# Kernel optimization log

Hardware: AMD Instinct MI355X
Metric: run time of the kernel (lower is better)

Reference implementation:

```python
import jax, jax.numpy as jnp
import numpy as np

LOSS_WEIGHT = 1.0

# Zero-padded shifts implementing PyTorch cross-correlation stencils.
# _shift_w(x, +1)[..., j] = x[..., j+1] (zero outside), etc.

def _shift_w(x, s):
    if s == 1:
        return jnp.pad(x[..., 1:], ((0, 0), (0, 0), (0, 1)))
    return jnp.pad(x[..., :-1], ((0, 0), (0, 0), (1, 0)))


def _shift_h(x, s):
    if s == 1:
        return jnp.pad(x[..., 1:, :], ((0, 0), (0, 1), (0, 0)))
    return jnp.pad(x[..., :-1, :], ((0, 0), (1, 0), (0, 0)))


def _curvature_loss(prob):
    # prob: [B, H, W]. Fused stencil chain equivalent to the 7 tiny conv2d calls.
    lap = (_shift_h(prob, 1) + _shift_h(prob, -1)
           + _shift_w(prob, 1) + _shift_w(prob, -1) - 4.0 * prob)
    gx = _shift_w(lap, 1) - _shift_w(lap, -1)          # dx = [-1, 0, 1]
    gy = _shift_h(lap, 1) - _shift_h(lap, -1)          # dy = [-1, 0, 1]^T
    hxx = 2.0 * gx - _shift_w(gx, 1) - _shift_w(gx, -1)  # dxx = [-1, 2, -1]
    hyy = 2.0 * gy - _shift_h(gy, 1) - _shift_h(gy, -1)  # dyy = [-1, 2, -1]^T
    hxy = _shift_w(gx, 1) - _shift_w(gx, -1)
    numerator = hxx * (1.0 + gy) ** 2 - 2.0 * hxy * gx * gy + hyy * (1.0 + gx) ** 2
    denominator = 2.0 * (1.0 + gx ** 2 + gy ** 2) ** 1.5
    curvature = numerator / denominator
    neg_curv = jnp.maximum(-curvature, 0.0)
    s = jnp.sum(neg_curv, axis=(1, 2))                              # [B]
    c = jnp.sum(neg_curv != 0, axis=(1, 2)).astype(prob.dtype)      # [B]
    # per-sample masked mean, skipped when no negative curvature
    per_sample = jnp.where(c > 0, s / jnp.maximum(c, 1.0), 0.0)
    return jnp.sum(per_sample)


def setup_inputs() -> dict:
    key = jax.random.key(0)
    k1, k2 = jax.random.split(key)
    pred = jax.random.normal(k1, (8, 4, 1024, 1024), dtype=jnp.float32)
    target = jax.random.randint(k2, (8, 1024, 1024), 0, 4, dtype=jnp.int64)
    return {"pred": pred, "target": target}


def reference(pred, target):
    # softmax=True path; num_classes == 4 branch of the original forward
    p = jax.nn.softmax(pred, axis=1)
    prob_1 = p[:, 1]
    prob_2 = p[:, 1] + p[:, 2]
    prob_3 = p[:, 3]
    loss = (_curvature_loss(prob_1) + _curvature_loss(prob_2)
            + _curvature_loss(prob_3))
    return loss * LOSS_WEIGHT
```

## Files before the change

### kernel.cpp

```cpp
#include <hip/hip_runtime.h>


namespace {
constexpr int H = 1024, W = 1024, B = 8;
constexpr int VALID = 120;
constexpr int NSTRIPS = 9;
constexpr int RCHUNK = 16;
constexpr int NCHUNKS = H / RCHUNK;
constexpr int WPB = 4;
constexpr int NTHREADS = 64 * WPB;
constexpr size_t HW = (size_t)H * W;
}

using v2f = __attribute__((ext_vector_type(2))) float;

__device__ __forceinline__ v2f mk2(float a, float b) {
    v2f r; r.x = a; r.y = b; return r;
}

__device__ __forceinline__ float dpp_left(float x) {
    return __builtin_bit_cast(float,
        __builtin_amdgcn_update_dpp(0, __builtin_bit_cast(int, x),
                                    0x138 , 0xf, 0xf, false));
}
__device__ __forceinline__ float dpp_right(float x) {
    return __builtin_bit_cast(float,
        __builtin_amdgcn_update_dpp(0, __builtin_bit_cast(int, x),
                                    0x130 , 0xf, 0xf, false));
}

__global__ void zero_ws_kernel(unsigned int* ws) {
    if (threadIdx.x < 48) ws[threadIdx.x] = 0u;
}

template <bool RE>
__device__ __forceinline__ void load_row4(const float* __restrict__ basep, int row,
                                          v2f o[4]) {
    const int rc = RE ? min(max(row, 0), H - 1) : row;
    const float* p = basep + (size_t)rc * W;
    o[0] = *(const v2f*)p;
    o[1] = *(const v2f*)(p + HW);
    o[2] = *(const v2f*)(p + 2 * HW);
    o[3] = *(const v2f*)(p + 3 * HW);
}

template <bool EDGE>
__device__ __forceinline__ void softmax_pair(const v2f x[4], bool ok0, bool ok1,
                                             v2f p[3]) {
    const float e0x = __expf(x[0].x), e1x = __expf(x[1].x);
    const float e2x = __expf(x[2].x), e3x = __expf(x[3].x);
    const float e0y = __expf(x[0].y), e1y = __expf(x[1].y);
    const float e2y = __expf(x[2].y), e3y = __expf(x[3].y);
    const float ix = __builtin_amdgcn_rcpf(e0x + e1x + e2x + e3x);
    const float iy = __builtin_amdgcn_rcpf(e0y + e1y + e2y + e3y);
    if (EDGE) {
        p[0] = mk2(ok0 ? e1x * ix : 0.f,          ok1 ? e1y * iy : 0.f);
        p[1] = mk2(ok0 ? (e1x + e2x) * ix : 0.f,  ok1 ? (e1y + e2y) * iy : 0.f);
        p[2] = mk2(ok0 ? e3x * ix : 0.f,          ok1 ? e3y * iy : 0.f);
    } else {
        p[0] = mk2(e1x * ix,          e1y * iy);
        p[1] = mk2((e1x + e2x) * ix,  (e1y + e2y) * iy);
        p[2] = mk2(e3x * ix,          e3y * iy);
    }
}

template <bool CE, bool RE>
__device__ __forceinline__ void sweep(const float* __restrict__ pred,
                                      int b, int strip, int chunk, int lane,
                                      v2f sacc[3], unsigned int cacc0[3],
                                      unsigned int cacc1[3]) {
    const int r0 = chunk * RCHUNK;
    const int li0 = 2 * lane;
    const int col0 = strip * VALID - 4 + li0;
    const int col1 = col0 + 1;
    const int colC = CE ? min(max(col0, 0), W - 2) : col0;
    const float* basep = pred + (size_t)b * 4 * HW + colC;

    const bool cOK0 = !CE || ((unsigned)col0 < (unsigned)W);
    const bool cOK1 = !CE || ((unsigned)col1 < (unsigned)W);
    const bool aOK0 = (li0 >= 4) && (li0 <= 123) && cOK0;
    const bool aOK1 = (li0 + 1 >= 4) && (li0 + 1 <= 123) && cOK1;
    const v2f aM = mk2(aOK0 ? 1.f : 0.f, aOK1 ? 1.f : 0.f);
    const v2f gxpM = mk2((!CE || (col0 + 1 < W)) ? 1.f : 0.f,
                         (!CE || (col1 + 1 < W)) ? 1.f : 0.f);
    const v2f gxmM = mk2((!CE || (col0 >= 1)) ? 1.f : 0.f,
                         (!CE || (col1 >= 1)) ? 1.f : 0.f);

    v2f P[5][3];
    v2f L[5][3];
    v2f Rr[2][4];

    {
        v2f t[4];
        load_row4<RE>(basep, r0 - 3, t);
        const bool ok = !RE || ((unsigned)(r0 - 3) < (unsigned)H);
        softmax_pair<CE || RE>(t, ok && cOK0, ok && cOK1, P[3]);
        load_row4<RE>(basep, r0 - 2, t);
        const bool ok2 = !RE || ((unsigned)(r0 - 2) < (unsigned)H);
        softmax_pair<CE || RE>(t, ok2 && cOK0, ok2 && cOK1, P[4]);
    }
    load_row4<RE>(basep, r0 - 1, Rr[0]);
    load_row4<RE>(basep, r0, Rr[1]);

    for (int m = 0; m < 2; ++m) {
#pragma unroll
        for (int u = 0; u < 10; ++u) {
            const int y = r0 - 4 + m * 10 + u;
            const bool pok = !RE || ((unsigned)(y + 3) < (unsigned)H);
            softmax_pair<CE || RE>(Rr[u % 2], pok && cOK0, pok && cOK1, P[u % 5]);
            load_row4<RE>(basep, y + 5, Rr[u % 2]);
            const bool lok = !RE || ((unsigned)(y + 2) < (unsigned)H);
#pragma unroll
            for (int f = 0; f < 3; ++f) {
                const v2f top = P[(u + 3) % 5][f];
                const v2f mid = P[(u + 4) % 5][f];
                const v2f bot = P[u % 5][f];
                const float lft = dpp_left(mid.y);
                const float rgt = dpp_right(mid.x);
                const v2f horiz = mk2(lft, mid.x) + mk2(mid.y, rgt);
                const v2f l = top + bot + horiz - 4.f * mid;
                if (CE || RE) {
                    L[u % 5][f] = mk2((lok && cOK0) ? l.x : 0.f,
                                      (lok && cOK1) ? l.y : 0.f);
                } else {
                    L[u % 5][f] = l;
                }
            }
            if (m > 0 || u >= 4) {
                const float gypM = (!RE || (y + 1 < H)) ? 1.f : 0.f;
                const float gymM = (!RE || (y >= 1)) ? 1.f : 0.f;
#pragma unroll
                for (int f = 0; f < 3; ++f) {
                    const v2f lm2 = L[(u + 1) % 5][f];
                    const v2f lm1 = L[(u + 2) % 5][f];
                    const v2f lc  = L[(u + 3) % 5][f];
                    const v2f lp1 = L[(u + 4) % 5][f];
                    const v2f lp2 = L[u % 5][f];
                    const float A  = dpp_left(lc.y);
                    const float Bm = dpp_left(lc.x);
                    const float Bp = dpp_right(lc.x);
                    const float Cc = dpp_right(lc.y);
                    const v2f c   = lc;
                    const v2f gx  = mk2(lc.y, Bp) - mk2(A, lc.x);
                    const v2f gy  = lp1 - lm1;
                    const v2f gxp = (mk2(Bp, Cc) - c) * gxpM;
                    const v2f gxm = (c - mk2(Bm, A)) * gxmM;
                    const v2f gyp = (lp2 - c) * gypM;
                    const v2f gym = (c - lm2) * gymM;
                    const v2f hxx = 2.f * gx - gxp - gxm;
                    const v2f hxy = gxp - gxm;
                    const v2f hyy = 2.f * gy - gyp - gym;
                    const v2f ox = 1.f + gx, oy = 1.f + gy;
                    const v2f numer = hxx * oy * oy - 2.f * hxy * (gx * gy)
                                    + hyy * ox * ox;
                    const v2f xx = 1.f + gx * gx + gy * gy;
                    const float rs0 = __builtin_amdgcn_rsqf(xx.x);
                    const float rs1 = __builtin_amdgcn_rsqf(xx.y);
                    const v2f invden = mk2(0.5f * rs0 * rs0 * rs0,
                                           0.5f * rs1 * rs1 * rs1);
                    const v2f curv = numer * invden;
                    const v2f negc = mk2(fmaxf(-curv.x, 0.f),
                                         fmaxf(-curv.y, 0.f)) * aM;
                    sacc[f] += negc;
                    cacc0[f] += (negc.x != 0.f) ? 1u : 0u;
                    cacc1[f] += (negc.y != 0.f) ? 1u : 0u;
                }
            }
        }
    }
}

__global__ __launch_bounds__(NTHREADS, 4)
void curvature_sweep(const float* __restrict__ pred,
                     float* __restrict__ s_ws,
                     unsigned int* __restrict__ c_ws) {
    __shared__ float redS[3][WPB];
    __shared__ unsigned int redC[3][WPB];

    const int strip = blockIdx.x;
    const int b = blockIdx.z;
    const int tid = threadIdx.x;
    const int wv = tid >> 6, lane = tid & 63;
    const int chunk = blockIdx.y * WPB + wv;

    const bool ce = (strip == 0) || (strip == NSTRIPS - 1);
    const bool re = (chunk == 0) || (chunk == NCHUNKS - 1);

    v2f sacc[3] = {mk2(0.f, 0.f), mk2(0.f, 0.f), mk2(0.f, 0.f)};
    unsigned int cacc0[3] = {0u, 0u, 0u};
    unsigned int cacc1[3] = {0u, 0u, 0u};
    if (!ce && !re)
        sweep<false, false>(pred, b, strip, chunk, lane, sacc, cacc0, cacc1);
    else if (ce && !re)
        sweep<true, false>(pred, b, strip, chunk, lane, sacc, cacc0, cacc1);
    else if (!ce && re)
        sweep<false, true>(pred, b, strip, chunk, lane, sacc, cacc0, cacc1);
    else
        sweep<true, true>(pred, b, strip, chunk, lane, sacc, cacc0, cacc1);

#pragma unroll
    for (int f = 0; f < 3; ++f) {
        float v = sacc[f].x + sacc[f].y;
        unsigned int c = cacc0[f] + cacc1[f];
        for (int off = 32; off > 0; off >>= 1) {
            v += __shfl_xor(v, off, 64);
            c += __shfl_xor(c, off, 64);
        }
        if (lane == 0) { redS[f][wv] = v; redC[f][wv] = c; }
    }
    __syncthreads();
    if (tid < 3) {
        float v = 0.f;
        unsigned int c = 0;
        for (int w2 = 0; w2 < WPB; ++w2) { v += redS[tid][w2]; c += redC[tid][w2]; }
        atomicAdd(&s_ws[b * 3 + tid], v);
        atomicAdd(&c_ws[b * 3 + tid], c);
    }
}

__global__ void finalize_kernel(const float* __restrict__ s_ws,
                                const unsigned int* __restrict__ c_ws,
                                float* __restrict__ out) {
    const int lane = threadIdx.x;
    float v = 0.f;
    if (lane < 24) {
        const float s = s_ws[lane];
        const unsigned int c = c_ws[lane];
        v = (c > 0) ? s / (float)c : 0.f;
    }
    for (int off = 32; off > 0; off >>= 1) v += __shfl_down(v, off, 64);
    if (lane == 0) out[0] = v;
}

extern "C" void kernel_launch(void* const* d_in, const int* in_sizes, int n_in,
                              void* d_out, int out_size, void* d_ws, size_t ws_size,
                              hipStream_t stream) {
    const float* pred = (const float*)d_in[0];
    float* s_ws = (float*)d_ws;
    unsigned int* c_ws = (unsigned int*)((char*)d_ws + 24 * sizeof(float));
    float* out = (float*)d_out;

    hipLaunchKernelGGL(zero_ws_kernel, dim3(1), dim3(64), 0, stream,
                       (unsigned int*)d_ws);
    dim3 grid(NSTRIPS, NCHUNKS / WPB, B);
    hipLaunchKernelGGL(curvature_sweep, grid, dim3(NTHREADS), 0, stream,
                       pred, s_ws, c_ws);
    hipLaunchKernelGGL(finalize_kernel, dim3(1), dim3(64), 0, stream,
                       s_ws, c_ws, out);
}
```

Measured before the change: 56.42 us.

## Deepen row prefetch, fully unroll sweep, and hoist per-pixel masking to reduction

Each wave now keeps four input rows in flight instead of two, and the row loop is fully unrolled over all 20 iterations instead of two partially unrolled halves of 10. The softmax ring buffer shrinks from five to four rows. The per-pixel valid-column mask multiply and the 0.5 factor are removed from the inner loop and applied once per lane before the wave reduction. This moves per-pixel ALU work out of the loop and hides more load latency, at the cost of more registers and a larger unrolled code body.

```diff
diff --git a/kernel.cpp b/kernel.cpp
--- a/kernel.cpp
+++ b/kernel.cpp
@@ -78,93 +78,89 @@
 
     const bool cOK0 = !CE || ((unsigned)col0 < (unsigned)W);
     const bool cOK1 = !CE || ((unsigned)col1 < (unsigned)W);
-    const bool aOK0 = (li0 >= 4) && (li0 <= 123) && cOK0;
-    const bool aOK1 = (li0 + 1 >= 4) && (li0 + 1 <= 123) && cOK1;
-    const v2f aM = mk2(aOK0 ? 1.f : 0.f, aOK1 ? 1.f : 0.f);
     const v2f gxpM = mk2((!CE || (col0 + 1 < W)) ? 1.f : 0.f,
                          (!CE || (col1 + 1 < W)) ? 1.f : 0.f);
     const v2f gxmM = mk2((!CE || (col0 >= 1)) ? 1.f : 0.f,
                          (!CE || (col1 >= 1)) ? 1.f : 0.f);
 
-    v2f P[5][3];
+    v2f P[4][3];
     v2f L[5][3];
-    v2f Rr[2][4];
+    v2f Rr[4][4];
 
     {
         v2f t[4];
         load_row4<RE>(basep, r0 - 3, t);
         const bool ok = !RE || ((unsigned)(r0 - 3) < (unsigned)H);
-        softmax_pair<CE || RE>(t, ok && cOK0, ok && cOK1, P[3]);
+        softmax_pair<CE || RE>(t, ok && cOK0, ok && cOK1, P[2]);
         load_row4<RE>(basep, r0 - 2, t);
         const bool ok2 = !RE || ((unsigned)(r0 - 2) < (unsigned)H);
-        softmax_pair<CE || RE>(t, ok2 && cOK0, ok2 && cOK1, P[4]);
+        softmax_pair<CE || RE>(t, ok2 && cOK0, ok2 && cOK1, P[3]);
     }
     load_row4<RE>(basep, r0 - 1, Rr[0]);
-    load_row4<RE>(basep, r0, Rr[1]);
-
-    for (int m = 0; m < 2; ++m) {
-#pragma unroll
-        for (int u = 0; u < 10; ++u) {
-            const int y = r0 - 4 + m * 10 + u;
-            const bool pok = !RE || ((unsigned)(y + 3) < (unsigned)H);
-            softmax_pair<CE || RE>(Rr[u % 2], pok && cOK0, pok && cOK1, P[u % 5]);
-            load_row4<RE>(basep, y + 5, Rr[u % 2]);
-            const bool lok = !RE || ((unsigned)(y + 2) < (unsigned)H);
+    load_row4<RE>(basep, r0 + 0, Rr[1]);
+    load_row4<RE>(basep, r0 + 1, Rr[2]);
+    load_row4<RE>(basep, r0 + 2, Rr[3]);
+
+#pragma unroll
+    for (int i = 0; i < RCHUNK + 4; ++i) {
+        const int y = r0 - 4 + i;
+        const bool pok = !RE || ((unsigned)(y + 3) < (unsigned)H);
+        softmax_pair<CE || RE>(Rr[i % 4], pok && cOK0, pok && cOK1, P[i % 4]);
+        if (i < RCHUNK) load_row4<RE>(basep, y + 7, Rr[i % 4]);
+        const bool lok = !RE || ((unsigned)(y + 2) < (unsigned)H);
+#pragma unroll
+        for (int f = 0; f < 3; ++f) {
+            const v2f top = P[(i + 2) % 4][f];
+            const v2f mid = P[(i + 3) % 4][f];
+            const v2f bot = P[i % 4][f];
+            const float lft = dpp_left(mid.y);
+            const float rgt = dpp_right(mid.x);
+            const v2f horiz = mk2(lft, mid.x) + mk2(mid.y, rgt);
+            const v2f l = top + bot + horiz - 4.f * mid;
+            if (CE || RE) {
+                L[i % 5][f] = mk2((lok && cOK0) ? l.x : 0.f,
+                                  (lok && cOK1) ? l.y : 0.f);
+            } else {
+                L[i % 5][f] = l;
+            }
+        }
+        if (i >= 4) {
+            const float gypM = (!RE || (y + 1 < H)) ? 1.f : 0.f;
+            const float gymM = (!RE || (y >= 1)) ? 1.f : 0.f;
 #pragma unroll
             for (int f = 0; f < 3; ++f) {
-                const v2f top = P[(u + 3) % 5][f];
-                const v2f mid = P[(u + 4) % 5][f];
-                const v2f bot = P[u % 5][f];
-                const float lft = dpp_left(mid.y);
-                const float rgt = dpp_right(mid.x);
-                const v2f horiz = mk2(lft, mid.x) + mk2(mid.y, rgt);
-                const v2f l = top + bot + horiz - 4.f * mid;
-                if (CE || RE) {
-                    L[u % 5][f] = mk2((lok && cOK0) ? l.x : 0.f,
-                                      (lok && cOK1) ? l.y : 0.f);
-                } else {
-                    L[u % 5][f] = l;
-                }
-            }
-            if (m > 0 || u >= 4) {
-                const float gypM = (!RE || (y + 1 < H)) ? 1.f : 0.f;
-                const float gymM = (!RE || (y >= 1)) ? 1.f : 0.f;
-#pragma unroll
-                for (int f = 0; f < 3; ++f) {
-                    const v2f lm2 = L[(u + 1) % 5][f];
-                    const v2f lm1 = L[(u + 2) % 5][f];
-                    const v2f lc  = L[(u + 3) % 5][f];
-                    const v2f lp1 = L[(u + 4) % 5][f];
-                    const v2f lp2 = L[u % 5][f];
-                    const float A  = dpp_left(lc.y);
-                    const float Bm = dpp_left(lc.x);
-                    const float Bp = dpp_right(lc.x);
-                    const float Cc = dpp_right(lc.y);
-                    const v2f c   = lc;
-                    const v2f gx  = mk2(lc.y, Bp) - mk2(A, lc.x);
-                    const v2f gy  = lp1 - lm1;
-                    const v2f gxp = (mk2(Bp, Cc) - c) * gxpM;
-                    const v2f gxm = (c - mk2(Bm, A)) * gxmM;
-                    const v2f gyp = (lp2 - c) * gypM;
-                    const v2f gym = (c - lm2) * gymM;
-                    const v2f hxx = 2.f * gx - gxp - gxm;
-                    const v2f hxy = gxp - gxm;
-                    const v2f hyy = 2.f * gy - gyp - gym;
-                    const v2f ox = 1.f + gx, oy = 1.f + gy;
-                    const v2f numer = hxx * oy * oy - 2.f * hxy * (gx * gy)
-                                    + hyy * ox * ox;
-                    const v2f xx = 1.f + gx * gx + gy * gy;
-                    const float rs0 = __builtin_amdgcn_rsqf(xx.x);
-                    const float rs1 = __builtin_amdgcn_rsqf(xx.y);
-                    const v2f invden = mk2(0.5f * rs0 * rs0 * rs0,
-                                           0.5f * rs1 * rs1 * rs1);
-                    const v2f curv = numer * invden;
-                    const v2f negc = mk2(fmaxf(-curv.x, 0.f),
-                                         fmaxf(-curv.y, 0.f)) * aM;
-                    sacc[f] += negc;
-                    cacc0[f] += (negc.x != 0.f) ? 1u : 0u;
-                    cacc1[f] += (negc.y != 0.f) ? 1u : 0u;
-                }
+                const v2f lm2 = L[(i + 1) % 5][f];
+                const v2f lm1 = L[(i + 2) % 5][f];
+                const v2f lc  = L[(i + 3) % 5][f];
+                const v2f lp1 = L[(i + 4) % 5][f];
+                const v2f lp2 = L[i % 5][f];
+                const float A  = dpp_left(lc.y);
+                const float Bm = dpp_left(lc.x);
+                const float Bp = dpp_right(lc.x);
+                const float Cc = dpp_right(lc.y);
+                const v2f c   = lc;
+                const v2f gx  = mk2(lc.y, Bp) - mk2(A, lc.x);
+                const v2f gy  = lp1 - lm1;
+                const v2f gxp = (mk2(Bp, Cc) - c) * gxpM;
+                const v2f gxm = (c - mk2(Bm, A)) * gxmM;
+                const v2f gyp = (lp2 - c) * gypM;
+                const v2f gym = (c - lm2) * gymM;
+                const v2f hxx = 2.f * gx - gxp - gxm;
+                const v2f hxy = gxp - gxm;
+                const v2f hyy = 2.f * gy - gyp - gym;
+                const v2f ox = 1.f + gx, oy = 1.f + gy;
+                const v2f numer = hxx * oy * oy - 2.f * hxy * (gx * gy)
+                                + hyy * ox * ox;
+                const v2f xx = 1.f + gx * gx + gy * gy;
+                const float rs0 = __builtin_amdgcn_rsqf(xx.x);
+                const float rs1 = __builtin_amdgcn_rsqf(xx.y);
+                const v2f invden2 = mk2(rs0 * rs0 * rs0, rs1 * rs1 * rs1);
+                const v2f curv2 = numer * invden2;
+                const v2f negc = mk2(fmaxf(-curv2.x, 0.f),
+                                     fmaxf(-curv2.y, 0.f));
+                sacc[f] += negc;
+                cacc0[f] += (negc.x != 0.f) ? 1u : 0u;
+                cacc1[f] += (negc.y != 0.f) ? 1u : 0u;
             }
         }
     }
@@ -198,10 +194,13 @@
     else
         sweep<true, true>(pred, b, strip, chunk, lane, sacc, cacc0, cacc1);
 
+    const int col0 = strip * VALID - 4 + 2 * lane;
+    const bool gOK = (lane >= 2) && (lane <= 61) && (col0 < W);
+
 #pragma unroll
     for (int f = 0; f < 3; ++f) {
-        float v = sacc[f].x + sacc[f].y;
-        unsigned int c = cacc0[f] + cacc1[f];
+        float v = gOK ? 0.5f * (sacc[f].x + sacc[f].y) : 0.f;
+        unsigned int c = gOK ? (cacc0[f] + cacc1[f]) : 0u;
         for (int off = 32; off > 0; off >>= 1) {
             v += __shfl_xor(v, off, 64);
             c += __shfl_xor(c, off, 64);
```

Result: no change. 56.55 us (+0.2%).
